# Optimization experiments

Hardware: AMD Instinct MI355X
Metric: run time of the kernel (lower is better)

## Reference

```python
import jax, jax.numpy as jnp
import numpy as np
import math

NHEADS = 4


def _mab(Q, K, qw, qb, kw, kb, vw, vb, ow, ob, mask):
    """MAB2 from tripletformer: multi-head attention (head split via cat(split,0)),
    softmax scale uses sqrt(FULL dim_V), masked_fill(mask==0, -1e10), residual on
    the projected Q, then O + relu(fc_o(O))."""
    dv = qw.shape[1]
    dh = dv // NHEADS
    B, Nq, _ = Q.shape
    Nk = K.shape[1]
    Qh = (Q @ qw + qb).reshape(B, Nq, NHEADS, dh).transpose(0, 2, 1, 3)  # B,h,Nq,dh
    Kh = (K @ kw + kb).reshape(B, Nk, NHEADS, dh).transpose(0, 2, 1, 3)
    Vh = (K @ vw + vb).reshape(B, Nk, NHEADS, dh).transpose(0, 2, 1, 3)
    att = jnp.einsum('bhqd,bhkd->bhqk', Qh, Kh) * (1.0 / math.sqrt(dv))
    att = jnp.where(mask, att, jnp.asarray(-1e10, att.dtype))
    A = jax.nn.softmax(att, axis=-1)
    Oh = Qh + jnp.einsum('bhqk,bhkd->bhqd', A, Vh)
    O = Oh.transpose(0, 2, 1, 3).reshape(B, Nq, dv)
    return O + jax.nn.relu(O @ ow + ob)


def _forward(context_x, value, mask, obs_len, iff_w, iff_b, ind_points,
             q0w, q0b, k0w, k0b, v0w, v0b, o0w, o0b,
             q1w, q1b, k1w, k1b, v1w, v1b, o1w, o1b):
    B, L = context_x.shape
    D = value.shape[-1]
    mflat = mask.reshape(B, L * D)
    # stable stream compaction: observed entries first, original (time-major,
    # channel-minor) order preserved; truncate to static obs_len
    order = jnp.argsort(-mflat, axis=-1, stable=True)[:, :obs_len]  # (B, N)
    T = jnp.broadcast_to(context_x[:, :, None], (B, L, D)).reshape(B, L * D)
    C = jnp.broadcast_to(jnp.arange(D, dtype=jnp.int32), (B, L, D)).reshape(B, L * D)
    U = value.reshape(B, L * D)
    take = lambda a: jnp.take_along_axis(a, order, axis=-1)
    T_, U_, mk_ = take(T), take(U), take(mflat)
    Ch = jax.nn.one_hot(take(C), D, dtype=value.dtype)  # one_hot(num_classes=dim-2)
    X = jnp.concatenate([Ch, T_[..., None], U_[..., None]], axis=-1) * mk_[..., None]
    Y = jax.nn.relu(X @ iff_w + iff_b) * mk_[..., None]
    key_valid = mk_ > 0                        # (B, N)
    mask1 = key_valid[:, None, None, :]        # mab0: mask padded keys
    mask2 = key_valid[:, None, :, None]        # mab1: mask padded query rows
    Z = Y
    n_layers = ind_points.shape[0]
    for i in range(n_layers):
        I = jnp.broadcast_to(ind_points[i], (B,) + ind_points[i].shape)
        H = _mab(I, Z, q0w[i], q0b[i], k0w[i], k0b[i], v0w[i], v0b[i], o0w[i], o0b[i], mask1)
        Zn = _mab(Z, H, q1w[i], q1b[i], k1w[i], k1b[i], v1w[i], v1b[i], o1w[i], o1b[i], mask2)
        Z = Zn * mk_[..., None] + Z
    return Z, mk_[..., None]


def setup_inputs() -> dict:
    B, L, D, OBS, DK, M, NL = 16, 512, 41, 4096, 128, 128, 3
    key = jax.random.key(0)
    ks = jax.random.split(key, 16)
    context_x = jnp.sort(jax.random.uniform(ks[0], (B, L), dtype=jnp.float32), axis=-1)
    value = jax.random.normal(ks[1], (B, L, D), dtype=jnp.float32)
    # exactly OBS observed entries per batch row -> static packed length
    r = jax.random.uniform(ks[2], (B, L * D))
    kth = jnp.sort(r, axis=-1)[:, OBS]
    mask = (r < kth[:, None]).astype(jnp.float32).reshape(B, L, D)

    def w(k, shape, fan):
        return jax.random.normal(k, shape, dtype=jnp.float32) / math.sqrt(fan)

    inp = dict(
        context_x=context_x, value=value, mask=mask, obs_len=OBS,
        iff_w=w(ks[3], (D + 2, DK), D + 2), iff_b=jnp.zeros((DK,), jnp.float32),
        ind_points=w(ks[4], (NL, M, DK), DK),
    )
    for j, n in enumerate(['q0', 'k0', 'v0', 'o0', 'q1', 'k1', 'v1', 'o1']):
        inp[n + 'w'] = w(ks[5 + j], (NL, DK, DK), DK)
        inp[n + 'b'] = jnp.zeros((NL, DK), jnp.float32)
    return inp


def reference(context_x, value, mask, obs_len, iff_w, iff_b, ind_points,
              q0w, q0b, k0w, k0b, v0w, v0b, o0w, o0b,
              q1w, q1b, k1w, k1b, v1w, v1b, o1w, o1b):
    return _forward(context_x, value, mask, obs_len, iff_w, iff_b, ind_points,
                    q0w, q0b, k0w, k0b, v0w, v0b, o0w, o0b,
                    q1w, q1b, k1w, k1b, v1w, v1b, o1w, o1b)
```

## Files before the change

kernel.cpp:

```cpp
#include <hip/hip_runtime.h>
#include <math.h>

#define NBATCH 16
#define SEQL   512
#define DIM    41
#define LDFLAT (SEQL*DIM)
#define OBS    4096
#define DK     128
#define NH     4
#define DH     32

typedef short bf16x8 __attribute__((ext_vector_type(8)));
typedef short short8v __attribute__((ext_vector_type(8)));
typedef float floatx4 __attribute__((ext_vector_type(4)));

__device__ __forceinline__ short f2bf(float f) {
  union { float f; unsigned u; } v;
  v.f = f;
  unsigned r = (v.u + 0x7fffu + ((v.u >> 16) & 1u)) >> 16;
  return (short)r;
}
__device__ __forceinline__ float bf2f(short s) {
  union { unsigned u; float f; } v;
  v.u = ((unsigned)(unsigned short)s) << 16;
  return v.f;
}


__device__ __forceinline__ int swz(int row, int col) {
  return row * 128 + ((((col >> 3) ^ row) & 15) << 3) + (col & 7);
}

typedef struct { int4 v[4]; } WStageH;
__device__ __forceinline__ void stage_load_h(WStageH& s,
                                             const short* __restrict__ Wh,
                                             int tid) {
#pragma unroll
  for (int k = 0; k < 4; k++)
    s.v[k] = *(const int4*)&Wh[(size_t)tid * 8 + (size_t)k * 2048];
}
__device__ __forceinline__ void stage_write_h(short* Wl, const WStageH& s,
                                              int tid) {
#pragma unroll
  for (int k = 0; k < 4; k++) {
    int i = tid * 8 + k * 2048;
    *(int4*)&Wl[swz(i >> 7, i & 127)] = s.v[k];
  }
}
typedef struct { int4 v[2]; } WStageF;
__device__ __forceinline__ void stage_load_f(WStageF& s,
                                             const short* __restrict__ W,
                                             int tid) {
#pragma unroll
  for (int k = 0; k < 2; k++)
    s.v[k] = *(const int4*)&W[(size_t)tid * 8 + (size_t)k * 8192];
}
__device__ __forceinline__ void stage_write_f(short* Wl, const WStageF& s,
                                              int tid) {
#pragma unroll
  for (int k = 0; k < 2; k++) {
    int i = tid * 8 + k * 8192;
    *(int4*)&Wl[swz(i >> 7, i & 127)] = s.v[k];
  }
}

__device__ __forceinline__ void gemm4_s(const short* Wl, const bf16x8 af[4],
                                        int lm, int quad, floatx4 acc[4]) {
#pragma unroll
  for (int nt = 0; nt < 4; nt++) acc[nt] = (floatx4){0.f, 0.f, 0.f, 0.f};
#pragma unroll
  for (int kc = 0; kc < 4; kc++) {
    bf16x8 a = af[kc];
#pragma unroll
    for (int nt = 0; nt < 4; nt++) {
      bf16x8 b = *(const bf16x8*)&Wl[swz(nt * 16 + lm, kc * 32 + quad * 8)];
      acc[nt] = __builtin_amdgcn_mfma_f32_16x16x32_bf16(a, b, acc[nt], 0, 0, 0);
    }
  }
}
__device__ __forceinline__ void gemm2_s(const short* Wl, const bf16x8 af[4],
                                        int colq, int lm, int quad,
                                        floatx4 acc[2]) {
#pragma unroll
  for (int nt = 0; nt < 2; nt++) acc[nt] = (floatx4){0.f, 0.f, 0.f, 0.f};
#pragma unroll
  for (int kc = 0; kc < 4; kc++) {
    bf16x8 a = af[kc];
#pragma unroll
    for (int nt = 0; nt < 2; nt++) {
      bf16x8 b = *(const bf16x8*)&Wl[swz(colq * 32 + nt * 16 + lm,
                                         kc * 32 + quad * 8)];
      acc[nt] = __builtin_amdgcn_mfma_f32_16x16x32_bf16(a, b, acc[nt], 0, 0, 0);
    }
  }
}
__device__ __forceinline__ void load_af_s(const short* Xl, int strip, int lm,
                                          int quad, bf16x8 af[4]) {
#pragma unroll
  for (int kc = 0; kc < 4; kc++)
    af[kc] = *(const bf16x8*)&Xl[swz(strip * 16 + lm, kc * 32 + quad * 8)];
}
__device__ __forceinline__ void store_sl4(short* Sl, const floatx4 acc[4],
                                          const float* __restrict__ bias,
                                          int wv, int lm, int quad,
                                          int colbase) {
#pragma unroll
  for (int nt = 0; nt < 4; nt++) {
    int col = colbase + nt * 16 + lm;
    float bn = bias[col];
#pragma unroll
    for (int r = 0; r < 4; r++)
      Sl[swz(wv * 16 + quad * 4 + r, col)] = f2bf(acc[nt][r] + bn);
  }
}
__device__ __forceinline__ void write_hs_s(const short* Sl,
                                           short* __restrict__ out, int rb,
                                           int nshift, int tid) {
  int rr = tid >> 2, hh = tid & 3;
  int r = rb + rr;
  int bb = r >> nshift, nn = r & ((1 << nshift) - 1);
  size_t o = (((size_t)(bb * NH + hh) << nshift) + nn) * 32;
#pragma unroll
  for (int j = 0; j < 4; j++)
    *(int4*)&out[o + j * 8] = *(int4*)&Sl[swz(rr, hh * 32 + j * 8)];
}
__device__ __forceinline__ void write_hs_q(const short* Sl,
                                           short* __restrict__ out, int rb,
                                           int nshift, int strip, int colq,
                                           int lane) {
  int rr = strip * 16 + (lane >> 2);
  int r = rb + rr;
  int bb = r >> nshift, nn = r & ((1 << nshift) - 1);
  size_t o = (((size_t)(bb * NH + colq) << nshift) + nn) * 32 + (lane & 3) * 8;
  *(int4*)&out[o] = *(const int4*)&Sl[swz(rr, colq * 32 + (lane & 3) * 8)];
}

__global__ __launch_bounds__(1024) void prep_build_kernel(
    const float* __restrict__ q0w, const float* __restrict__ k0w,
    const float* __restrict__ v0w, const float* __restrict__ o0w,
    const float* __restrict__ q1w, const float* __restrict__ k1w,
    const float* __restrict__ v1w, const float* __restrict__ o1w,
    short* __restrict__ Wt,
    const float* __restrict__ mask, int* __restrict__ order,
    float* __restrict__ mk_out, float* __restrict__ mk_out2) {
  __shared__ float Tl[128 * 132];
  __shared__ int wsums[16];
  __shared__ int s_total_ones;
  __shared__ int s_chunk_ones;
  __shared__ int s_ones_base;
  __shared__ int s_zeros_base;
  int tid = threadIdx.x;

  if (blockIdx.x < 24) {
    int id = blockIdx.x, l = id >> 3, wi = id & 7;
    const float* s;
    switch (wi) {
      case 0: s = q0w; break; case 1: s = k0w; break;
      case 2: s = v0w; break; case 3: s = o0w; break;
      case 4: s = q1w; break; case 5: s = k1w; break;
      case 6: s = v1w; break; default: s = o1w; break;
    }
    s += (size_t)l * 16384;
    for (int i = tid * 4; i < 16384; i += 4096) {
      int k = i >> 7, n = i & 127;
      float4 x = *(const float4*)&s[i];
      Tl[k * 132 + n + 0] = x.x; Tl[k * 132 + n + 1] = x.y;
      Tl[k * 132 + n + 2] = x.z; Tl[k * 132 + n + 3] = x.w;
    }
    __syncthreads();
    short* dst = Wt + (size_t)id * 16384;
    int n = tid >> 3, k0 = (tid & 7) * 16;
    for (int jc = 0; jc < 2; jc++) {
      short8v t;
#pragma unroll
      for (int j = 0; j < 8; j++) t[j] = f2bf(Tl[(k0 + jc * 8 + j) * 132 + n]);
      *(short8v*)&dst[n * 128 + k0 + jc * 8] = t;
    }
    return;
  }

  int b = blockIdx.x - 24;
  const float* m = mask + (size_t)b * LDFLAT;
  int lane = tid & 63, w = tid >> 6;

  int cnt = 0;
  for (int j = tid; j < LDFLAT; j += 1024) cnt += (m[j] > 0.f) ? 1 : 0;
  for (int off = 32; off > 0; off >>= 1) cnt += __shfl_xor(cnt, off);
  if (lane == 0) wsums[w] = cnt;
  __syncthreads();
  if (tid == 0) {
    int t = 0;
    for (int i = 0; i < 16; i++) t += wsums[i];
    s_total_ones = t; s_ones_base = 0; s_zeros_base = 0;
  }
  __syncthreads();
  int total_ones = s_total_ones;

  for (int c0 = 0; c0 < LDFLAT; c0 += 1024) {
    __syncthreads();
    int j = c0 + tid;
    bool valid = (j < LDFLAT);
    float mv = valid ? m[j] : 0.f;
    int one = (valid && mv > 0.f) ? 1 : 0;
    int v = one;
    for (int off = 1; off < 64; off <<= 1) {
      int t = __shfl_up(v, (unsigned)off);
      if (lane >= off) v += t;
    }
    if (lane == 63) wsums[w] = v;
    __syncthreads();
    if (tid == 0) {
      int run = 0;
      for (int i = 0; i < 16; i++) { int t = wsums[i]; wsums[i] = run; run += t; }
      s_chunk_ones = run;
    }
    __syncthreads();
    int ones_before = (v - one) + wsums[w];
    int ob = s_ones_base, zb = s_zeros_base, chunk_ones = s_chunk_ones;
    int rem = LDFLAT - c0;
    int chunk_valid = rem < 1024 ? rem : 1024;
    int valid_before = tid < rem ? tid : rem;
    if (valid) {
      int pos = one ? (ob + ones_before)
                    : (total_ones + zb + (valid_before - ones_before));
      if (pos < OBS) {
        order[b * OBS + pos] = j;
        mk_out[b * OBS + pos] = mv;
        mk_out2[b * OBS + pos] = mv;
      }
    }
    __syncthreads();
    if (tid == 0) {
      s_ones_base = ob + chunk_ones;
      s_zeros_base = zb + (chunk_valid - chunk_ones);
    }
  }
}

__global__ __launch_bounds__(256, 3) void fusedA_kernel(
    const int* __restrict__ order, const float* __restrict__ mk_g,
    const float* __restrict__ cx, const float* __restrict__ value,
    const float* __restrict__ iff_w, const float* __restrict__ iff_b,
    float* __restrict__ Z,
    const short* __restrict__ Wk, const float* __restrict__ kbias,
    short* __restrict__ Kb,
    const short* __restrict__ Wv, const float* __restrict__ vbias,
    short* __restrict__ Vb,
    const short* __restrict__ Wq, const float* __restrict__ qbias,
    short* __restrict__ Qb,
    const float* __restrict__ indp, const short* __restrict__ WtAll,
    const float* __restrict__ q0b_all, short* __restrict__ qh_b) {
  __shared__ __align__(16) short Xl[64 * 128];
  __shared__ __align__(16) short WlA[64 * 128];
  __shared__ __align__(16) short WlB[64 * 128];
  int tid = threadIdx.x;
  int wv = tid >> 6, lane = tid & 63, lm = lane & 15, quad = lane >> 4;
  int r_l = lane >> 2, seg = lane & 3;
  int lrow = wv * 16 + r_l;

  if (blockIdx.x >= 1024) {
    int id = blockIdx.x - 1024;
    int l = id >> 1, rbq = (id & 1) * 64;
    const float* X = indp + (size_t)l * 16384 + (size_t)rbq * 128;
    const short* W = WtAll + (size_t)(l * 8) * 16384;
    const float* bias = q0b_all + (size_t)l * 128;
    short* out = qh_b + (size_t)l * 16384;
    WStageH sA, sB;
    stage_load_h(sA, W, tid);
    stage_load_h(sB, W + 8192, tid);
    const float* Xr = X + (size_t)lrow * 128;
#pragma unroll
    for (int jj = 0; jj < 8; jj++) {
      int col = seg * 32 + jj * 4;
      float4 x = *(const float4*)&Xr[col];
      *(short4*)&Xl[swz(lrow, col)] =
          make_short4(f2bf(x.x), f2bf(x.y), f2bf(x.z), f2bf(x.w));
    }
    stage_write_h(WlA, sA, tid);
    stage_write_h(WlB, sB, tid);
    __syncthreads();
    bf16x8 af[4];
    load_af_s(Xl, wv, lm, quad, af);
    floatx4 acc[4];
    gemm4_s(WlA, af, lm, quad, acc);
    store_sl4(Xl, acc, bias, wv, lm, quad, 0);
    gemm4_s(WlB, af, lm, quad, acc);
    store_sl4(Xl, acc, bias, wv, lm, quad, 64);
    write_hs_s(Xl, out, rbq, 7, tid);
    return;
  }

  int rb = blockIdx.x * 64;
  WStageH s0; stage_load_h(s0, Wk, tid);
  int grow = rb + lrow;
  int bb = grow >> 12;
  int j = order[grow];
  int l = j / DIM, d = j - l * DIM;
  float t = cx[bb * SEQL + l];
  float u = value[(size_t)bb * LDFLAT + j];
  float mkv = mk_g[grow];
#pragma unroll
  for (int jj = 0; jj < 8; jj++) {
    int col = seg * 32 + jj * 4;
    float4 w0 = *(const float4*)&iff_w[d * DK + col];
    float4 w1 = *(const float4*)&iff_w[41 * DK + col];
    float4 w2 = *(const float4*)&iff_w[42 * DK + col];
    float4 b4 = *(const float4*)&iff_b[col];
    float4 z;
    z.x = fmaxf(w0.x + t * w1.x + u * w2.x + b4.x, 0.f) * mkv;
    z.y = fmaxf(w0.y + t * w1.y + u * w2.y + b4.y, 0.f) * mkv;
    z.z = fmaxf(w0.z + t * w1.z + u * w2.z + b4.z, 0.f) * mkv;
    z.w = fmaxf(w0.w + t * w1.w + u * w2.w + b4.w, 0.f) * mkv;
    *(float4*)&Z[(size_t)grow * DK + col] = z;
    *(short4*)&Xl[swz(lrow, col)] =
        make_short4(f2bf(z.x), f2bf(z.y), f2bf(z.z), f2bf(z.w));
  }
  stage_write_h(WlA, s0, tid);
  __syncthreads();
  WStageH s1; stage_load_h(s1, Wk + 8192, tid);
  bf16x8 af[4];
  load_af_s(Xl, wv, lm, quad, af);
  floatx4 acc[4];
  gemm4_s(WlA, af, lm, quad, acc);
  store_sl4(Xl, acc, kbias, wv, lm, quad, 0);
  stage_write_h(WlB, s1, tid);
  __syncthreads();
  WStageH s2; stage_load_h(s2, Wv, tid);
  gemm4_s(WlB, af, lm, quad, acc);
  store_sl4(Xl, acc, kbias, wv, lm, quad, 64);
  write_hs_s(Xl, Kb, rb, 12, tid);
  stage_write_h(WlA, s2, tid);
  __syncthreads();
  WStageH s3; stage_load_h(s3, Wv + 8192, tid);
  gemm4_s(WlA, af, lm, quad, acc);
  store_sl4(Xl, acc, vbias, wv, lm, quad, 0);
  stage_write_h(WlB, s3, tid);
  __syncthreads();
  WStageH s4; stage_load_h(s4, Wq, tid);
  gemm4_s(WlB, af, lm, quad, acc);
  store_sl4(Xl, acc, vbias, wv, lm, quad, 64);
  write_hs_s(Xl, Vb, rb, 12, tid);
  stage_write_h(WlA, s4, tid);
  __syncthreads();
  WStageH s5; stage_load_h(s5, Wq + 8192, tid);
  gemm4_s(WlA, af, lm, quad, acc);
  store_sl4(Xl, acc, qbias, wv, lm, quad, 0);
  stage_write_h(WlB, s5, tid);
  __syncthreads();
  gemm4_s(WlB, af, lm, quad, acc);
  store_sl4(Xl, acc, qbias, wv, lm, quad, 64);
  write_hs_s(Xl, Qb, rb, 12, tid);
}

__global__ __launch_bounds__(256) void attn1_kernel(
    const short* __restrict__ Qh,
    const short* __restrict__ Kh, const short* __restrict__ Vh,
    const float* __restrict__ mk,
    float* __restrict__ Opart, float* __restrict__ mpart,
    float* __restrict__ lpart) {
  __shared__ __align__(16) short Ql[128 * 40];
  __shared__ __align__(16) short Kc[64 * 40];
  __shared__ __align__(16) short Vtc[32 * 74];
  __shared__ __align__(16) short Pl[128 * 72];
  __shared__ float mkc[64];
  int bh = blockIdx.x;
  int b = bh >> 2, h = bh & 3;
  int ks = blockIdx.y;
  int tid = threadIdx.x;
  int wv = tid >> 6, lane = tid & 63, lm = lane & 15, quad = lane >> 4;

  const float scale = 0.08838834764831845f;
  const short* kbase = Kh + ((size_t)bh * OBS + ks * 512) * 32;
  const short* vbase = Vh + ((size_t)bh * OBS + ks * 512) * 32;
  const float* mkb = mk + (size_t)b * OBS + ks * 512;

  int i0 = tid * 8;
  int r0 = i0 >> 5, cv = i0 & 31;
  int4 kreg = *(const int4*)&kbase[i0];
  int4 vreg = *(const int4*)&vbase[i0];
  float mreg = (tid < 64) ? mkb[tid] : 0.f;

  const short* qbg = Qh + (size_t)h * 128 * 32;
  for (int i = tid * 8; i < 128 * 32; i += 2048) {
    int r = i >> 5, c = i & 31;
    *(int4*)&Ql[r * 40 + c] = *(const int4*)&qbg[i];
  }
  __syncthreads();
  bf16x8 aq[2];
  aq[0] = *(bf16x8*)&Ql[(wv * 32 + lm) * 40 + quad * 8];
  aq[1] = *(bf16x8*)&Ql[(wv * 32 + 16 + lm) * 40 + quad * 8];

  float m_i[2][4], l_i[2][4];
  floatx4 oacc[2][2];
#pragma unroll
  for (int mt = 0; mt < 2; mt++) {
#pragma unroll
    for (int r = 0; r < 4; r++) { m_i[mt][r] = -1e30f; l_i[mt][r] = 0.f; }
    oacc[mt][0] = (floatx4){0.f, 0.f, 0.f, 0.f};
    oacc[mt][1] = (floatx4){0.f, 0.f, 0.f, 0.f};
  }

  for (int ch = 0; ch < 8; ch++) {
    __syncthreads();
    *(int4*)&Kc[r0 * 40 + cv] = kreg;
    {
      short* vv = (short*)&vreg;
#pragma unroll
      for (int j = 0; j < 8; j++) Vtc[(cv + j) * 74 + r0] = vv[j];
    }
    if (tid < 64) mkc[tid] = mreg;
    if (ch < 7) {
      kreg = *(const int4*)&kbase[(ch + 1) * 2048 + i0];
      vreg = *(const int4*)&vbase[(ch + 1) * 2048 + i0];
      if (tid < 64) mreg = mkb[(ch + 1) * 64 + tid];
    }
    __syncthreads();

    floatx4 sf[2][4];
#pragma unroll
    for (int nt = 0; nt < 4; nt++) {
      bf16x8 bfrag = *(bf16x8*)&Kc[(nt * 16 + lm) * 40 + quad * 8];
      floatx4 z = {0.f, 0.f, 0.f, 0.f};
      sf[0][nt] = __builtin_amdgcn_mfma_f32_16x16x32_bf16(aq[0], bfrag, z, 0, 0, 0);
      sf[1][nt] = __builtin_amdgcn_mfma_f32_16x16x32_bf16(aq[1], bfrag, z, 0, 0, 0);
    }
#pragma unroll
    for (int nt = 0; nt < 4; nt++) {
      float mkv = mkc[nt * 16 + lm];
      bool ok = mkv > 0.f;
#pragma unroll
      for (int mt = 0; mt < 2; mt++)
#pragma unroll
        for (int r = 0; r < 4; r++)
          sf[mt][nt][r] = ok ? sf[mt][nt][r] * scale : -1e10f;
    }
#pragma unroll
    for (int mt = 0; mt < 2; mt++) {
#pragma unroll
      for (int r = 0; r < 4; r++) {
        float mx = fmaxf(fmaxf(sf[mt][0][r], sf[mt][1][r]),
                         fmaxf(sf[mt][2][r], sf[mt][3][r]));
        mx = fmaxf(mx, __shfl_xor(mx, 1));
        mx = fmaxf(mx, __shfl_xor(mx, 2));
        mx = fmaxf(mx, __shfl_xor(mx, 4));
        mx = fmaxf(mx, __shfl_xor(mx, 8));
        float mn = fmaxf(m_i[mt][r], mx);
        float al = __expf(m_i[mt][r] - mn);
        float ps = 0.f;
#pragma unroll
        for (int nt = 0; nt < 4; nt++) {
          float p = __expf(sf[mt][nt][r] - mn);
          sf[mt][nt][r] = p;
          ps += p;
        }
        ps += __shfl_xor(ps, 1);
        ps += __shfl_xor(ps, 2);
        ps += __shfl_xor(ps, 4);
        ps += __shfl_xor(ps, 8);
        l_i[mt][r] = l_i[mt][r] * al + ps;
        m_i[mt][r] = mn;
        oacc[mt][0] *= al;
        oacc[mt][1] *= al;
      }
    }
#pragma unroll
    for (int mt = 0; mt < 2; mt++)
#pragma unroll
      for (int nt = 0; nt < 4; nt++)
#pragma unroll
        for (int r = 0; r < 4; r++)
          Pl[(wv * 32 + mt * 16 + quad * 4 + r) * 72 + nt * 16 + lm] =
              f2bf(sf[mt][nt][r]);
#pragma unroll
    for (int kc = 0; kc < 2; kc++) {
      bf16x8 vf0 = *(bf16x8*)&Vtc[lm * 74 + kc * 32 + quad * 8];
      bf16x8 vf1 = *(bf16x8*)&Vtc[(16 + lm) * 74 + kc * 32 + quad * 8];
#pragma unroll
      for (int mt = 0; mt < 2; mt++) {
        bf16x8 pf = *(bf16x8*)&Pl[(wv * 32 + mt * 16 + lm) * 72 + kc * 32 + quad * 8];
        oacc[mt][0] = __builtin_amdgcn_mfma_f32_16x16x32_bf16(pf, vf0, oacc[mt][0], 0, 0, 0);
        oacc[mt][1] = __builtin_amdgcn_mfma_f32_16x16x32_bf16(pf, vf1, oacc[mt][1], 0, 0, 0);
      }
    }
  }
  float* ob = Opart + (size_t)(ks * 64 + bh) * 128 * 32;
#pragma unroll
  for (int mt = 0; mt < 2; mt++) {
#pragma unroll
    for (int r = 0; r < 4; r++) {
      int row = wv * 32 + mt * 16 + quad * 4 + r;
      ob[(size_t)row * 32 + lm] = oacc[mt][0][r];
      ob[(size_t)row * 32 + 16 + lm] = oacc[mt][1][r];
      if (lm == 0) {
        mpart[(size_t)(ks * 64 + bh) * 128 + row] = m_i[mt][r];
        lpart[(size_t)(ks * 64 + bh) * 128 + row] = l_i[mt][r];
      }
    }
  }
}

__global__ __launch_bounds__(1024) void fusedB_kernel(
    const float* __restrict__ Opart, const float* __restrict__ mpart,
    const float* __restrict__ lpart, const short* __restrict__ qh,
    const short* __restrict__ Wo, const float* __restrict__ obias,
    const short* __restrict__ Wk, const float* __restrict__ kbias,
    const short* __restrict__ Wv, const float* __restrict__ vbias,
    short* __restrict__ khb, short* __restrict__ vhb) {
  __shared__ __align__(16) short Xl[64 * 128];
  __shared__ __align__(16) short WlA[128 * 128];
  __shared__ __align__(16) short WlB[128 * 128];
  int tid = threadIdx.x;
  int rb = blockIdx.x * 64;
  int b = rb >> 7, n0 = rb & 127;
  int wv = tid >> 6, lane = tid & 63, lm = lane & 15, quad = lane >> 4;
  int strip = wv & 3, colq = wv >> 2;
  WStageF sWo; stage_load_f(sWo, Wo, tid);
#pragma unroll
  for (int p = 0; p < 2; p++) {
    int slot = p * 1024 + tid;
    int pair = slot >> 3;
    int hh = pair & 3, rr = pair >> 2;
    int c4 = (slot & 7) * 4;
    int n = n0 + rr;
    int bh = b * 4 + hh;
    float mv[8], lv[8], m = -1e30f;
#pragma unroll
    for (int s = 0; s < 8; s++) {
      mv[s] = mpart[(size_t)(s * 64 + bh) * 128 + n];
      lv[s] = lpart[(size_t)(s * 64 + bh) * 128 + n];
      m = fmaxf(m, mv[s]);
    }
    float l = 0.f, oa0 = 0.f, oa1 = 0.f, oa2 = 0.f, oa3 = 0.f;
#pragma unroll
    for (int s = 0; s < 8; s++) {
      float w = __expf(mv[s] - m);
      l += lv[s] * w;
      float4 v = *(const float4*)&Opart[((size_t)(s * 64 + bh) * 128 + n) * 32 + c4];
      oa0 += v.x * w; oa1 += v.y * w; oa2 += v.z * w; oa3 += v.w * w;
    }
    float li = 1.f / l;
    int2 qi = *(const int2*)&qh[((size_t)hh * 128 + n) * 32 + c4];
    const short* qs = (const short*)&qi;
    short4 o4;
    o4.x = f2bf(bf2f(qs[0]) + oa0 * li);
    o4.y = f2bf(bf2f(qs[1]) + oa1 * li);
    o4.z = f2bf(bf2f(qs[2]) + oa2 * li);
    o4.w = f2bf(bf2f(qs[3]) + oa3 * li);
    *(short4*)&Xl[swz(rr, hh * 32 + c4)] = o4;
  }
  stage_write_f(WlA, sWo, tid);
  __syncthreads();
  bf16x8 afO[4];
  load_af_s(Xl, strip, lm, quad, afO);
  __syncthreads();
  WStageF sWk; stage_load_f(sWk, Wk, tid);
  floatx4 acc[2];
  gemm2_s(WlA, afO, colq, lm, quad, acc);
#pragma unroll
  for (int nt = 0; nt < 2; nt++) {
    int col = colq * 32 + nt * 16 + lm;
    float bn = obias[col];
#pragma unroll
    for (int r = 0; r < 4; r++) {
      int row = strip * 16 + quad * 4 + r;
      float ov = bf2f(Xl[swz(row, col)]);
      Xl[swz(row, col)] = f2bf(ov + fmaxf(acc[nt][r] + bn, 0.f));
    }
  }
  stage_write_f(WlB, sWk, tid);
  __syncthreads();
  bf16x8 afH[4];
  load_af_s(Xl, strip, lm, quad, afH);
  __syncthreads();
  WStageF sWv; stage_load_f(sWv, Wv, tid);
  gemm2_s(WlB, afH, colq, lm, quad, acc);
#pragma unroll
  for (int nt = 0; nt < 2; nt++) {
    int col = colq * 32 + nt * 16 + lm;
    float bn = kbias[col];
#pragma unroll
    for (int r = 0; r < 4; r++)
      Xl[swz(strip * 16 + quad * 4 + r, col)] = f2bf(acc[nt][r] + bn);
  }
  write_hs_q(Xl, khb, rb, 7, strip, colq, lane);
  stage_write_f(WlA, sWv, tid);
  __syncthreads();
  gemm2_s(WlA, afH, colq, lm, quad, acc);
#pragma unroll
  for (int nt = 0; nt < 2; nt++) {
    int col = colq * 32 + nt * 16 + lm;
    float bn = vbias[col];
#pragma unroll
    for (int r = 0; r < 4; r++)
      Xl[swz(strip * 16 + quad * 4 + r, col)] = f2bf(acc[nt][r] + bn);
  }
  write_hs_q(Xl, vhb, rb, 7, strip, colq, lane);
}

__global__ __launch_bounds__(256) void attn2_kernel(
    const short* __restrict__ Qh, const short* __restrict__ Kh,
    const short* __restrict__ Vh, short* __restrict__ O) {
  __shared__ __align__(16) short Kl[128 * 40];
  __shared__ __align__(16) short Vt[32 * 136];
  __shared__ __align__(16) short Ql[64 * 40];
  __shared__ __align__(16) short Pl[64 * 136];
  int bh = blockIdx.x;
  int b = bh >> 2, h = bh & 3;
  int q0 = blockIdx.y * 64;
  int tid = threadIdx.x;
  int wv = tid >> 6, lane = tid & 63, lm = lane & 15, quad = lane >> 4;
  const short* kb = Kh + (size_t)bh * 128 * 32;
  const short* vb = Vh + (size_t)bh * 128 * 32;
  const short* qb = Qh + ((size_t)bh * OBS + q0) * 32;

  for (int i = tid * 8; i < 128 * 32; i += 2048) {
    int r = i >> 5, c = i & 31;
    *(int4*)&Kl[r * 40 + c] = *(const int4*)&kb[i];
  }
  for (int i = tid * 8; i < 64 * 32; i += 2048) {
    int r = i >> 5, c = i & 31;
    *(int4*)&Ql[r * 40 + c] = *(const int4*)&qb[i];
  }
  for (int i = tid * 8; i < 128 * 32; i += 2048) {
    int r = i >> 5, c = i & 31;
    int4 vv4 = *(const int4*)&vb[i];
    short* vv = (short*)&vv4;
#pragma unroll
    for (int j = 0; j < 8; j++) Vt[(c + j) * 136 + r] = vv[j];
  }
  __syncthreads();

  const float scale = 0.08838834764831845f;
  bf16x8 afrag = *(bf16x8*)&Ql[(wv * 16 + lm) * 40 + quad * 8];
  floatx4 sf[8];
#pragma unroll
  for (int nt = 0; nt < 8; nt++) {
    bf16x8 bfrag = *(bf16x8*)&Kl[(nt * 16 + lm) * 40 + quad * 8];
    floatx4 z = {0.f, 0.f, 0.f, 0.f};
    sf[nt] = __builtin_amdgcn_mfma_f32_16x16x32_bf16(afrag, bfrag, z, 0, 0, 0);
  }
#pragma unroll
  for (int nt = 0; nt < 8; nt++) sf[nt] *= scale;
  float linv[4];
#pragma unroll
  for (int r = 0; r < 4; r++) {
    float mx = sf[0][r];
#pragma unroll
    for (int nt = 1; nt < 8; nt++) mx = fmaxf(mx, sf[nt][r]);
    mx = fmaxf(mx, __shfl_xor(mx, 1));
    mx = fmaxf(mx, __shfl_xor(mx, 2));
    mx = fmaxf(mx, __shfl_xor(mx, 4));
    mx = fmaxf(mx, __shfl_xor(mx, 8));
    float sum = 0.f;
#pragma unroll
    for (int nt = 0; nt < 8; nt++) {
      float p = __expf(sf[nt][r] - mx);
      sf[nt][r] = p;
      sum += p;
    }
    sum += __shfl_xor(sum, 1);
    sum += __shfl_xor(sum, 2);
    sum += __shfl_xor(sum, 4);
    sum += __shfl_xor(sum, 8);
    linv[r] = 1.f / sum;
  }
#pragma unroll
  for (int nt = 0; nt < 8; nt++)
#pragma unroll
    for (int r = 0; r < 4; r++)
      Pl[(wv * 16 + quad * 4 + r) * 136 + nt * 16 + lm] = f2bf(sf[nt][r]);

  floatx4 oacc[2] = {{0.f, 0.f, 0.f, 0.f}, {0.f, 0.f, 0.f, 0.f}};
#pragma unroll
  for (int kc = 0; kc < 4; kc++) {
    bf16x8 pf = *(bf16x8*)&Pl[(wv * 16 + lm) * 136 + kc * 32 + quad * 8];
#pragma unroll
    for (int nt2 = 0; nt2 < 2; nt2++) {
      bf16x8 vf = *(bf16x8*)&Vt[(nt2 * 16 + lm) * 136 + kc * 32 + quad * 8];
      oacc[nt2] = __builtin_amdgcn_mfma_f32_16x16x32_bf16(pf, vf, oacc[nt2], 0, 0, 0);
    }
  }
  short* Ol = Pl;
#pragma unroll
  for (int nt2 = 0; nt2 < 2; nt2++) {
#pragma unroll
    for (int r = 0; r < 4; r++) {
      int qrow = wv * 16 + quad * 4 + r;
      float q = bf2f(Ql[qrow * 40 + nt2 * 16 + lm]);
      Ol[qrow * 136 + nt2 * 16 + lm] = f2bf(q + oacc[nt2][r] * linv[r]);
    }
  }
  int rr = tid >> 2, seg = tid & 3;
  size_t o = ((size_t)b * OBS + q0 + rr) * 128 + h * 32 + seg * 8;
  *(int4*)&O[o] = *(int4*)&Ol[rr * 136 + seg * 8];
}

__global__ __launch_bounds__(256, 3) void fusedC_kernel(
    const short* __restrict__ Ob, const short* __restrict__ Wo,
    const float* __restrict__ obias, const float* __restrict__ mk,
    const float* __restrict__ Zin, float* __restrict__ Zout,
    const short* __restrict__ Wk, const float* __restrict__ kbias,
    short* __restrict__ Kb,
    const short* __restrict__ Wv, const float* __restrict__ vbias,
    short* __restrict__ Vb,
    const short* __restrict__ Wq, const float* __restrict__ qbias,
    short* __restrict__ Qb) {
  __shared__ __align__(16) short Xl[64 * 128];
  __shared__ __align__(16) short WlA[64 * 128];
  __shared__ __align__(16) short WlB[64 * 128];
  int tid = threadIdx.x;
  int rb = blockIdx.x * 64;
  int wv = tid >> 6, lane = tid & 63, lm = lane & 15, quad = lane >> 4;

  WStageH s0; stage_load_h(s0, Wo, tid);
  bf16x8 afO[4];
  {
    const short* arow = Ob + (size_t)(rb + wv * 16 + lm) * 128;
#pragma unroll
    for (int kc = 0; kc < 4; kc++) {
      afO[kc] = *(const bf16x8*)&arow[kc * 32 + quad * 8];
      *(bf16x8*)&Xl[swz(wv * 16 + lm, kc * 32 + quad * 8)] = afO[kc];
    }
  }
  int row0 = wv * 16 + quad * 4;
  float mkv[4];
#pragma unroll
  for (int r = 0; r < 4; r++) mkv[r] = mk[rb + row0 + r];
  stage_write_h(WlA, s0, tid);
  __syncthreads();
  WStageH s1; stage_load_h(s1, Wo + 8192, tid);
  floatx4 acc[4];
  gemm4_s(WlA, afO, lm, quad, acc);
#pragma unroll
  for (int nt = 0; nt < 4; nt++) {
    int col = nt * 16 + lm;
    float bn = obias[col];
#pragma unroll
    for (int r = 0; r < 4; r++) {
      int row = row0 + r;
      size_t g = (size_t)(rb + row) * 128 + col;
      float ov = bf2f(Xl[swz(row, col)]);
      float f = ov + fmaxf(acc[nt][r] + bn, 0.f);
      float zv = Zin[g] + f * mkv[r];
      Zout[g] = zv;
      Xl[swz(row, col)] = f2bf(zv);
    }
  }
  stage_write_h(WlB, s1, tid);
  __syncthreads();
  WStageH s2;
  if (Wk) stage_load_h(s2, Wk, tid);
  gemm4_s(WlB, afO, lm, quad, acc);
#pragma unroll
  for (int nt = 0; nt < 4; nt++) {
    int col = 64 + nt * 16 + lm;
    float bn = obias[col];
#pragma unroll
    for (int r = 0; r < 4; r++) {
      int row = row0 + r;
      size_t g = (size_t)(rb + row) * 128 + col;
      float ov = bf2f(Xl[swz(row, col)]);
      float f = ov + fmaxf(acc[nt][r] + bn, 0.f);
      float zv = Zin[g] + f * mkv[r];
      Zout[g] = zv;
      Xl[swz(row, col)] = f2bf(zv);
    }
  }
  if (Wk == nullptr) return;
  bf16x8 af[4];
  load_af_s(Xl, wv, lm, quad, af);
  stage_write_h(WlA, s2, tid);
  __syncthreads();
  WStageH s3; stage_load_h(s3, Wk + 8192, tid);
  gemm4_s(WlA, af, lm, quad, acc);
  store_sl4(Xl, acc, kbias, wv, lm, quad, 0);
  stage_write_h(WlB, s3, tid);
  __syncthreads();
  WStageH s4; stage_load_h(s4, Wv, tid);
  gemm4_s(WlB, af, lm, quad, acc);
  store_sl4(Xl, acc, kbias, wv, lm, quad, 64);
  write_hs_s(Xl, Kb, rb, 12, tid);
  stage_write_h(WlA, s4, tid);
  __syncthreads();
  WStageH s5; stage_load_h(s5, Wv + 8192, tid);
  gemm4_s(WlA, af, lm, quad, acc);
  store_sl4(Xl, acc, vbias, wv, lm, quad, 0);
  stage_write_h(WlB, s5, tid);
  __syncthreads();
  WStageH s6; stage_load_h(s6, Wq, tid);
  gemm4_s(WlB, af, lm, quad, acc);
  store_sl4(Xl, acc, vbias, wv, lm, quad, 64);
  write_hs_s(Xl, Vb, rb, 12, tid);
  stage_write_h(WlA, s6, tid);
  __syncthreads();
  WStageH s7; stage_load_h(s7, Wq + 8192, tid);
  gemm4_s(WlA, af, lm, quad, acc);
  store_sl4(Xl, acc, qbias, wv, lm, quad, 0);
  stage_write_h(WlB, s7, tid);
  __syncthreads();
  gemm4_s(WlB, af, lm, quad, acc);
  store_sl4(Xl, acc, qbias, wv, lm, quad, 64);
  write_hs_s(Xl, Qb, rb, 12, tid);
}

extern "C" void kernel_launch(void* const* d_in, const int* in_sizes, int n_in,
                              void* d_out, int out_size, void* d_ws,
                              size_t ws_size, hipStream_t stream) {
  const float* cx    = (const float*)d_in[0];
  const float* value = (const float*)d_in[1];
  const float* mask  = (const float*)d_in[2];
  const float* iff_w = (const float*)d_in[4];
  const float* iff_b = (const float*)d_in[5];
  const float* indp  = (const float*)d_in[6];
  const float* q0w = (const float*)d_in[7];  const float* q0b = (const float*)d_in[8];
  const float* k0w = (const float*)d_in[9];  const float* k0b = (const float*)d_in[10];
  const float* v0w = (const float*)d_in[11]; const float* v0b = (const float*)d_in[12];
  const float* o0w = (const float*)d_in[13]; const float* o0b = (const float*)d_in[14];
  const float* q1w = (const float*)d_in[15]; const float* q1b = (const float*)d_in[16];
  const float* k1w = (const float*)d_in[17]; const float* k1b = (const float*)d_in[18];
  const float* v1w = (const float*)d_in[19]; const float* v1b = (const float*)d_in[20];
  const float* o1w = (const float*)d_in[21]; const float* o1b = (const float*)d_in[22];

  char* ws = (char*)d_ws;
  short* Wt    = (short*)ws;  ws += (size_t)24 * 16384 * 2;
  int*   order = (int*)ws;    ws += (size_t)NBATCH * OBS * 4;
  float* mk_g  = (float*)ws;  ws += (size_t)NBATCH * OBS * 4;
  float* Z     = (float*)ws;  ws += (size_t)NBATCH * OBS * DK * 4;
  short* Qb    = (short*)ws;  ws += (size_t)NBATCH * OBS * DK * 2;
  short* Kb    = (short*)ws;  ws += (size_t)NBATCH * OBS * DK * 2;
  short* Vb    = (short*)ws;  ws += (size_t)NBATCH * OBS * DK * 2;
  short* Ob    = (short*)ws;  ws += (size_t)NBATCH * OBS * DK * 2;
  short* qh_b  = (short*)ws;  ws += (size_t)3 * 128 * DK * 2;
  short* khb   = (short*)ws;  ws += (size_t)NBATCH * NH * 128 * DH * 2;
  short* vhb   = (short*)ws;  ws += (size_t)NBATCH * NH * 128 * DH * 2;
  float* Opart = (float*)ws;  ws += (size_t)8 * 64 * 128 * 32 * 4;
  float* mpart = (float*)ws;  ws += (size_t)8 * 64 * 128 * 4;
  float* lpart = (float*)ws;  ws += (size_t)8 * 64 * 128 * 4;

  float* outZ  = (float*)d_out;
  float* outMk = outZ + (size_t)NBATCH * OBS * DK;

  prep_build_kernel<<<40, 1024, 0, stream>>>(q0w, k0w, v0w, o0w, q1w, k1w,
                                             v1w, o1w, Wt, mask, order, mk_g,
                                             outMk);

  const short* W[3][8];
  for (int l = 0; l < 3; l++)
    for (int wi = 0; wi < 8; wi++) W[l][wi] = Wt + (size_t)(l * 8 + wi) * 16384;

  fusedA_kernel<<<1030, 256, 0, stream>>>(
      order, mk_g, cx, value, iff_w, iff_b, Z,
      W[0][1], k0b, Kb, W[0][2], v0b, Vb, W[0][4], q1b, Qb,
      indp, Wt, q0b, qh_b);

  for (int l = 0; l < 3; l++) {
    attn1_kernel<<<dim3(64, 8), 256, 0, stream>>>(
        qh_b + (size_t)l * 16384, Kb, Vb, mk_g, Opart, mpart, lpart);
    fusedB_kernel<<<32, 1024, 0, stream>>>(
        Opart, mpart, lpart, qh_b + (size_t)l * 16384,
        W[l][3], o0b + (size_t)l * 128,
        W[l][5], k1b + (size_t)l * 128,
        W[l][6], v1b + (size_t)l * 128, khb, vhb);
    attn2_kernel<<<dim3(64, 64), 256, 0, stream>>>(Qb, khb, vhb, Ob);
    if (l < 2) {
      fusedC_kernel<<<1024, 256, 0, stream>>>(
          Ob, W[l][7], o1b + (size_t)l * 128, mk_g, Z, Z,
          W[l + 1][1], k0b + (size_t)(l + 1) * 128, Kb,
          W[l + 1][2], v0b + (size_t)(l + 1) * 128, Vb,
          W[l + 1][4], q1b + (size_t)(l + 1) * 128, Qb);
    } else {
      fusedC_kernel<<<1024, 256, 0, stream>>>(
          Ob, W[l][7], o1b + (size_t)l * 128, mk_g, Z, outZ,
          nullptr, nullptr, nullptr, nullptr, nullptr, nullptr,
          nullptr, nullptr, nullptr);
    }
  }
}
```

Baseline: 458.2 us.

## Defer K/V head-split writes in registers and run K/V projections concurrently

In the embed and Z-update kernels, the K and V projection results are now packed into registers as bf16 pairs instead of being staged through shared memory and written out right away. They are unpacked and written to global memory at the end, after the Q projection. This removes shared-memory round trips and the global stores that sat between GEMM stages. In fusedB, the K and V weights are loaded together, and half the waves compute K while the other half compute V in parallel, using a second shared-memory output buffer. That removes one sequential weight-staging/GEMM phase and a barrier, at the cost of more registers, more LDS and wider per-wave output tiles.

```diff
diff --git a/kernel.cpp b/kernel.cpp
--- a/kernel.cpp
+++ b/kernel.cpp
@@ -94,6 +94,22 @@
     }
   }
 }
+__device__ __forceinline__ void gemm4_half(const short* Wl, const bf16x8 af[4],
+                                           int half, int lm, int quad,
+                                           floatx4 acc[4]) {
+#pragma unroll
+  for (int nt = 0; nt < 4; nt++) acc[nt] = (floatx4){0.f, 0.f, 0.f, 0.f};
+#pragma unroll
+  for (int kc = 0; kc < 4; kc++) {
+    bf16x8 a = af[kc];
+#pragma unroll
+    for (int nt = 0; nt < 4; nt++) {
+      bf16x8 b = *(const bf16x8*)&Wl[swz(half * 64 + nt * 16 + lm,
+                                         kc * 32 + quad * 8)];
+      acc[nt] = __builtin_amdgcn_mfma_f32_16x16x32_bf16(a, b, acc[nt], 0, 0, 0);
+    }
+  }
+}
 __device__ __forceinline__ void load_af_s(const short* Xl, int strip, int lm,
                                           int quad, bf16x8 af[4]) {
 #pragma unroll
@@ -111,6 +127,34 @@
 #pragma unroll
     for (int r = 0; r < 4; r++)
       Sl[swz(wv * 16 + quad * 4 + r, col)] = f2bf(acc[nt][r] + bn);
+  }
+}
+typedef struct { unsigned v[8]; } Pack8;
+__device__ __forceinline__ void pack8(Pack8& p, const floatx4 acc[4],
+                                      const float* __restrict__ bias,
+                                      int lm, int colbase) {
+#pragma unroll
+  for (int nt = 0; nt < 4; nt++) {
+    float bn = bias[colbase + nt * 16 + lm];
+#pragma unroll
+    for (int r = 0; r < 2; r++) {
+      unsigned lo = (unsigned)(unsigned short)f2bf(acc[nt][2 * r] + bn);
+      unsigned hi = (unsigned)(unsigned short)f2bf(acc[nt][2 * r + 1] + bn);
+      p.v[nt * 2 + r] = lo | (hi << 16);
+    }
+  }
+}
+__device__ __forceinline__ void unpack8(short* Sl, const Pack8& p, int wv,
+                                        int lm, int quad, int colbase) {
+#pragma unroll
+  for (int nt = 0; nt < 4; nt++) {
+    int col = colbase + nt * 16 + lm;
+#pragma unroll
+    for (int r = 0; r < 2; r++) {
+      unsigned w = p.v[nt * 2 + r];
+      Sl[swz(wv * 16 + quad * 4 + 2 * r, col)] = (short)(w & 0xffff);
+      Sl[swz(wv * 16 + quad * 4 + 2 * r + 1, col)] = (short)(w >> 16);
+    }
   }
 }
 __device__ __forceinline__ void write_hs_s(const short* Sl,
@@ -123,16 +167,6 @@
 #pragma unroll
   for (int j = 0; j < 4; j++)
     *(int4*)&out[o + j * 8] = *(int4*)&Sl[swz(rr, hh * 32 + j * 8)];
-}
-__device__ __forceinline__ void write_hs_q(const short* Sl,
-                                           short* __restrict__ out, int rb,
-                                           int nshift, int strip, int colq,
-                                           int lane) {
-  int rr = strip * 16 + (lane >> 2);
-  int r = rb + rr;
-  int bb = r >> nshift, nn = r & ((1 << nshift) - 1);
-  size_t o = (((size_t)(bb * NH + colq) << nshift) + nn) * 32 + (lane & 3) * 8;
-  *(int4*)&out[o] = *(const int4*)&Sl[swz(rr, colq * 32 + (lane & 3) * 8)];
 }
 
 __global__ __launch_bounds__(1024) void prep_build_kernel(
@@ -321,25 +355,24 @@
   bf16x8 af[4];
   load_af_s(Xl, wv, lm, quad, af);
   floatx4 acc[4];
+  Pack8 kp0, kp1, vp0, vp1;
   gemm4_s(WlA, af, lm, quad, acc);
-  store_sl4(Xl, acc, kbias, wv, lm, quad, 0);
+  pack8(kp0, acc, kbias, lm, 0);
   stage_write_h(WlB, s1, tid);
   __syncthreads();
   WStageH s2; stage_load_h(s2, Wv, tid);
   gemm4_s(WlB, af, lm, quad, acc);
-  store_sl4(Xl, acc, kbias, wv, lm, quad, 64);
-  write_hs_s(Xl, Kb, rb, 12, tid);
+  pack8(kp1, acc, kbias, lm, 64);
   stage_write_h(WlA, s2, tid);
   __syncthreads();
   WStageH s3; stage_load_h(s3, Wv + 8192, tid);
   gemm4_s(WlA, af, lm, quad, acc);
-  store_sl4(Xl, acc, vbias, wv, lm, quad, 0);
+  pack8(vp0, acc, vbias, lm, 0);
   stage_write_h(WlB, s3, tid);
   __syncthreads();
   WStageH s4; stage_load_h(s4, Wq, tid);
   gemm4_s(WlB, af, lm, quad, acc);
-  store_sl4(Xl, acc, vbias, wv, lm, quad, 64);
-  write_hs_s(Xl, Vb, rb, 12, tid);
+  pack8(vp1, acc, vbias, lm, 64);
   stage_write_h(WlA, s4, tid);
   __syncthreads();
   WStageH s5; stage_load_h(s5, Wq + 8192, tid);
@@ -350,6 +383,12 @@
   gemm4_s(WlB, af, lm, quad, acc);
   store_sl4(Xl, acc, qbias, wv, lm, quad, 64);
   write_hs_s(Xl, Qb, rb, 12, tid);
+  unpack8(Xl, kp0, wv, lm, quad, 0);
+  unpack8(Xl, kp1, wv, lm, quad, 64);
+  write_hs_s(Xl, Kb, rb, 12, tid);
+  unpack8(Xl, vp0, wv, lm, quad, 0);
+  unpack8(Xl, vp1, wv, lm, quad, 64);
+  write_hs_s(Xl, Vb, rb, 12, tid);
 }
 
 __global__ __launch_bounds__(256) void attn1_kernel(
@@ -507,6 +546,7 @@
     const short* __restrict__ Wv, const float* __restrict__ vbias,
     short* __restrict__ khb, short* __restrict__ vhb) {
   __shared__ __align__(16) short Xl[64 * 128];
+  __shared__ __align__(16) short Xl2[64 * 128];
   __shared__ __align__(16) short WlA[128 * 128];
   __shared__ __align__(16) short WlB[128 * 128];
   int tid = threadIdx.x;
@@ -514,6 +554,7 @@
   int b = rb >> 7, n0 = rb & 127;
   int wv = tid >> 6, lane = tid & 63, lm = lane & 15, quad = lane >> 4;
   int strip = wv & 3, colq = wv >> 2;
+  int half = (wv >> 2) & 1, which = wv >> 3;
   WStageF sWo; stage_load_f(sWo, Wo, tid);
 #pragma unroll
   for (int p = 0; p < 2; p++) {
@@ -553,9 +594,14 @@
   bf16x8 afO[4];
   load_af_s(Xl, strip, lm, quad, afO);
   __syncthreads();
-  WStageF sWk; stage_load_f(sWk, Wk, tid);
-  floatx4 acc[2];
-  gemm2_s(WlA, afO, colq, lm, quad, acc);
+  int t2 = tid & 511;
+  const short* Wp = (tid < 512) ? Wk : Wv;
+  int4 pw[4];
+#pragma unroll
+  for (int k = 0; k < 4; k++)
+    pw[k] = *(const int4*)&Wp[(size_t)t2 * 8 + (size_t)k * 4096];
+  floatx4 acc2[2];
+  gemm2_s(WlA, afO, colq, lm, quad, acc2);
 #pragma unroll
   for (int nt = 0; nt < 2; nt++) {
     int col = colq * 32 + nt * 16 + lm;
@@ -564,37 +610,45 @@
     for (int r = 0; r < 4; r++) {
       int row = strip * 16 + quad * 4 + r;
       float ov = bf2f(Xl[swz(row, col)]);
-      Xl[swz(row, col)] = f2bf(ov + fmaxf(acc[nt][r] + bn, 0.f));
-    }
-  }
-  stage_write_f(WlB, sWk, tid);
+      Xl[swz(row, col)] = f2bf(ov + fmaxf(acc2[nt][r] + bn, 0.f));
+    }
+  }
   __syncthreads();
   bf16x8 afH[4];
   load_af_s(Xl, strip, lm, quad, afH);
-  __syncthreads();
-  WStageF sWv; stage_load_f(sWv, Wv, tid);
-  gemm2_s(WlB, afH, colq, lm, quad, acc);
-#pragma unroll
-  for (int nt = 0; nt < 2; nt++) {
-    int col = colq * 32 + nt * 16 + lm;
-    float bn = kbias[col];
+  {
+    short* Wdst = (tid < 512) ? WlB : WlA;
+#pragma unroll
+    for (int k = 0; k < 4; k++) {
+      int i = t2 * 8 + k * 4096;
+      *(int4*)&Wdst[swz(i >> 7, i & 127)] = pw[k];
+    }
+  }
+  __syncthreads();
+  const short* Wl = which ? WlA : WlB;
+  const float* bp = which ? vbias : kbias;
+  short* Sdst = which ? Xl2 : Xl;
+  short* outp = which ? vhb : khb;
+  floatx4 acc[4];
+  gemm4_half(Wl, afH, half, lm, quad, acc);
+#pragma unroll
+  for (int nt = 0; nt < 4; nt++) {
+    int col = half * 64 + nt * 16 + lm;
+    float bn = bp[col];
 #pragma unroll
     for (int r = 0; r < 4; r++)
-      Xl[swz(strip * 16 + quad * 4 + r, col)] = f2bf(acc[nt][r] + bn);
-  }
-  write_hs_q(Xl, khb, rb, 7, strip, colq, lane);
-  stage_write_f(WlA, sWv, tid);
-  __syncthreads();
-  gemm2_s(WlA, afH, colq, lm, quad, acc);
-#pragma unroll
-  for (int nt = 0; nt < 2; nt++) {
-    int col = colq * 32 + nt * 16 + lm;
-    float bn = vbias[col];
-#pragma unroll
-    for (int r = 0; r < 4; r++)
-      Xl[swz(strip * 16 + quad * 4 + r, col)] = f2bf(acc[nt][r] + bn);
-  }
-  write_hs_q(Xl, vhb, rb, 7, strip, colq, lane);
+      Sdst[swz(strip * 16 + quad * 4 + r, col)] = f2bf(acc[nt][r] + bn);
+  }
+#pragma unroll
+  for (int j = 0; j < 2; j++) {
+    int rr = strip * 16 + (lane >> 2);
+    int hh = half * 2 + ((lane & 3) >> 1);
+    int s = (lane & 1) * 2 + j;
+    int r = rb + rr;
+    int bb2 = r >> 7, nn = r & 127;
+    size_t o = (((size_t)(bb2 * NH + hh) << 7) + nn) * 32 + s * 8;
+    *(int4*)&outp[o] = *(const int4*)&Sdst[swz(rr, hh * 32 + s * 8)];
+  }
 }
 
 __global__ __launch_bounds__(256) void attn2_kernel(
@@ -769,28 +823,27 @@
   if (Wk == nullptr) return;
   bf16x8 af[4];
   load_af_s(Xl, wv, lm, quad, af);
+  Pack8 kp0, kp1, vp0, vp1;
   stage_write_h(WlA, s2, tid);
   __syncthreads();
   WStageH s3; stage_load_h(s3, Wk + 8192, tid);
   gemm4_s(WlA, af, lm, quad, acc);
-  store_sl4(Xl, acc, kbias, wv, lm, quad, 0);
+  pack8(kp0, acc, kbias, lm, 0);
   stage_write_h(WlB, s3, tid);
   __syncthreads();
   WStageH s4; stage_load_h(s4, Wv, tid);
   gemm4_s(WlB, af, lm, quad, acc);
-  store_sl4(Xl, acc, kbias, wv, lm, quad, 64);
-  write_hs_s(Xl, Kb, rb, 12, tid);
+  pack8(kp1, acc, kbias, lm, 64);
   stage_write_h(WlA, s4, tid);
   __syncthreads();
   WStageH s5; stage_load_h(s5, Wv + 8192, tid);
   gemm4_s(WlA, af, lm, quad, acc);
-  store_sl4(Xl, acc, vbias, wv, lm, quad, 0);
+  pack8(vp0, acc, vbias, lm, 0);
   stage_write_h(WlB, s5, tid);
   __syncthreads();
   WStageH s6; stage_load_h(s6, Wq, tid);
   gemm4_s(WlB, af, lm, quad, acc);
-  store_sl4(Xl, acc, vbias, wv, lm, quad, 64);
-  write_hs_s(Xl, Vb, rb, 12, tid);
+  pack8(vp1, acc, vbias, lm, 64);
   stage_write_h(WlA, s6, tid);
   __syncthreads();
   WStageH s7; stage_load_h(s7, Wq + 8192, tid);
@@ -801,6 +854,12 @@
   gemm4_s(WlB, af, lm, quad, acc);
   store_sl4(Xl, acc, qbias, wv, lm, quad, 64);
   write_hs_s(Xl, Qb, rb, 12, tid);
+  unpack8(Xl, kp0, wv, lm, quad, 0);
+  unpack8(Xl, kp1, wv, lm, quad, 64);
+  write_hs_s(Xl, Kb, rb, 12, tid);
+  unpack8(Xl, vp0, wv, lm, quad, 0);
+  unpack8(Xl, vp1, wv, lm, quad, 64);
+  write_hs_s(Xl, Vb, rb, 12, tid);
 }
 
 extern "C" void kernel_launch(void* const* d_in, const int* in_sizes, int n_in,
```

New measurement: 512.9 us. +11.9%, slower.

## Parallelize mask compaction per-wave chunks and swizzle attention P buffer

Applied to the files above, without the earlier changes.

The stream-compaction part of prep_build_kernel is restructured. Each wave now counts and scans its own 1024-element chunk independently, using per-chunk prefix bases that a single thread computes once. This removes the roughly 21 sequential block-wide passes, each with several __syncthreads. The attention kernel also stores its P/O scratch in a swizzled 128-wide layout instead of padded 136 rows, and adds a minimum-occupancy launch bound of 4, aiming for less LDS use and higher occupancy, at some risk of extra register pressure.

```diff
diff --git a/kernel.cpp b/kernel.cpp
--- a/kernel.cpp
+++ b/kernel.cpp
@@ -144,11 +144,10 @@
     const float* __restrict__ mask, int* __restrict__ order,
     float* __restrict__ mk_out, float* __restrict__ mk_out2) {
   __shared__ float Tl[128 * 132];
-  __shared__ int wsums[16];
-  __shared__ int s_total_ones;
-  __shared__ int s_chunk_ones;
-  __shared__ int s_ones_base;
-  __shared__ int s_zeros_base;
+  __shared__ int c_ones[21];
+  __shared__ int base_ones[21];
+  __shared__ int base_zeros[21];
+  __shared__ int s_total;
   int tid = threadIdx.x;
 
   if (blockIdx.x < 24) {
@@ -183,56 +182,55 @@
   const float* m = mask + (size_t)b * LDFLAT;
   int lane = tid & 63, w = tid >> 6;
 
-  int cnt = 0;
-  for (int j = tid; j < LDFLAT; j += 1024) cnt += (m[j] > 0.f) ? 1 : 0;
-  for (int off = 32; off > 0; off >>= 1) cnt += __shfl_xor(cnt, off);
-  if (lane == 0) wsums[w] = cnt;
+  for (int ch = w; ch < 21; ch += 16) {
+    int cnt = 0;
+    for (int off = lane; off < 1024; off += 64) {
+      int j = ch * 1024 + off;
+      if (j < LDFLAT) cnt += (m[j] > 0.f) ? 1 : 0;
+    }
+    for (int o = 32; o > 0; o >>= 1) cnt += __shfl_xor(cnt, o);
+    if (lane == 0) c_ones[ch] = cnt;
+  }
   __syncthreads();
   if (tid == 0) {
-    int t = 0;
-    for (int i = 0; i < 16; i++) t += wsums[i];
-    s_total_ones = t; s_ones_base = 0; s_zeros_base = 0;
-  }
-  __syncthreads();
-  int total_ones = s_total_ones;
-
-  for (int c0 = 0; c0 < LDFLAT; c0 += 1024) {
-    __syncthreads();
-    int j = c0 + tid;
-    bool valid = (j < LDFLAT);
-    float mv = valid ? m[j] : 0.f;
-    int one = (valid && mv > 0.f) ? 1 : 0;
-    int v = one;
-    for (int off = 1; off < 64; off <<= 1) {
-      int t = __shfl_up(v, (unsigned)off);
-      if (lane >= off) v += t;
-    }
-    if (lane == 63) wsums[w] = v;
-    __syncthreads();
-    if (tid == 0) {
-      int run = 0;
-      for (int i = 0; i < 16; i++) { int t = wsums[i]; wsums[i] = run; run += t; }
-      s_chunk_ones = run;
-    }
-    __syncthreads();
-    int ones_before = (v - one) + wsums[w];
-    int ob = s_ones_base, zb = s_zeros_base, chunk_ones = s_chunk_ones;
-    int rem = LDFLAT - c0;
-    int chunk_valid = rem < 1024 ? rem : 1024;
-    int valid_before = tid < rem ? tid : rem;
-    if (valid) {
-      int pos = one ? (ob + ones_before)
-                    : (total_ones + zb + (valid_before - ones_before));
-      if (pos < OBS) {
-        order[b * OBS + pos] = j;
-        mk_out[b * OBS + pos] = mv;
-        mk_out2[b * OBS + pos] = mv;
+    int ro = 0, rz = 0, tot = 0;
+    for (int ch = 0; ch < 21; ch++) tot += c_ones[ch];
+    for (int ch = 0; ch < 21; ch++) {
+      base_ones[ch] = ro; base_zeros[ch] = rz;
+      int cv = (ch == 20) ? (LDFLAT - 20 * 1024) : 1024;
+      ro += c_ones[ch]; rz += cv - c_ones[ch];
+    }
+    s_total = tot;
+  }
+  __syncthreads();
+  int total_ones = s_total;
+  for (int ch = w; ch < 21; ch += 16) {
+    int obase = base_ones[ch], zbase = base_zeros[ch];
+    int climit = (ch == 20) ? (LDFLAT - 20 * 1024) : 1024;
+    int run_ones = 0;
+    for (int off0 = 0; off0 < climit; off0 += 64) {
+      int off = off0 + lane;
+      bool valid = off < climit;
+      int j = ch * 1024 + off;
+      float mv = valid ? m[j] : 0.f;
+      int one = (valid && mv > 0.f) ? 1 : 0;
+      int v = one;
+      for (int o = 1; o < 64; o <<= 1) {
+        int t = __shfl_up(v, (unsigned)o);
+        if (lane >= o) v += t;
       }
-    }
-    __syncthreads();
-    if (tid == 0) {
-      s_ones_base = ob + chunk_ones;
-      s_zeros_base = zb + (chunk_valid - chunk_ones);
+      int wave_ones = __shfl(v, 63);
+      if (valid) {
+        int ones_before = run_ones + (v - one);
+        int pos = one ? (obase + ones_before)
+                      : (total_ones + zbase + (off - ones_before));
+        if (pos < OBS) {
+          order[b * OBS + pos] = j;
+          mk_out[b * OBS + pos] = mv;
+          mk_out2[b * OBS + pos] = mv;
+        }
+      }
+      run_ones += wave_ones;
     }
   }
 }
@@ -597,13 +595,13 @@
   write_hs_q(Xl, vhb, rb, 7, strip, colq, lane);
 }
 
-__global__ __launch_bounds__(256) void attn2_kernel(
+__global__ __launch_bounds__(256, 4) void attn2_kernel(
     const short* __restrict__ Qh, const short* __restrict__ Kh,
     const short* __restrict__ Vh, short* __restrict__ O) {
   __shared__ __align__(16) short Kl[128 * 40];
   __shared__ __align__(16) short Vt[32 * 136];
   __shared__ __align__(16) short Ql[64 * 40];
-  __shared__ __align__(16) short Pl[64 * 136];
+  __shared__ __align__(16) short Pl[64 * 128];
   int bh = blockIdx.x;
   int b = bh >> 2, h = bh & 3;
   int q0 = blockIdx.y * 64;
@@ -668,12 +666,12 @@
   for (int nt = 0; nt < 8; nt++)
 #pragma unroll
     for (int r = 0; r < 4; r++)
-      Pl[(wv * 16 + quad * 4 + r) * 136 + nt * 16 + lm] = f2bf(sf[nt][r]);
+      Pl[swz(wv * 16 + quad * 4 + r, nt * 16 + lm)] = f2bf(sf[nt][r]);
 
   floatx4 oacc[2] = {{0.f, 0.f, 0.f, 0.f}, {0.f, 0.f, 0.f, 0.f}};
 #pragma unroll
   for (int kc = 0; kc < 4; kc++) {
-    bf16x8 pf = *(bf16x8*)&Pl[(wv * 16 + lm) * 136 + kc * 32 + quad * 8];
+    bf16x8 pf = *(bf16x8*)&Pl[swz(wv * 16 + lm, kc * 32 + quad * 8)];
 #pragma unroll
     for (int nt2 = 0; nt2 < 2; nt2++) {
       bf16x8 vf = *(bf16x8*)&Vt[(nt2 * 16 + lm) * 136 + kc * 32 + quad * 8];
@@ -687,12 +685,12 @@
     for (int r = 0; r < 4; r++) {
       int qrow = wv * 16 + quad * 4 + r;
       float q = bf2f(Ql[qrow * 40 + nt2 * 16 + lm]);
-      Ol[qrow * 136 + nt2 * 16 + lm] = f2bf(q + oacc[nt2][r] * linv[r]);
+      Ol[swz(qrow, nt2 * 16 + lm)] = f2bf(q + oacc[nt2][r] * linv[r]);
     }
   }
   int rr = tid >> 2, seg = tid & 3;
   size_t o = ((size_t)b * OBS + q0 + rr) * 128 + h * 32 + seg * 8;
-  *(int4*)&O[o] = *(int4*)&Ol[rr * 136 + seg * 8];
+  *(int4*)&O[o] = *(int4*)&Ol[swz(rr, seg * 8)];
 }
 
 __global__ __launch_bounds__(256, 3) void fusedC_kernel(
```

Result: no change. 459.8 us (+0.3%).
